# Optimization experiments

Hardware: AMD Instinct MI355X
Metric: run time of the kernel (lower is better)

Reference implementation:

```python
import jax, jax.numpy as jnp
import numpy as np

B, O, T, C_IN, IMG, P, D = 16, 3, 8, 3, 224, 16, 768
HF = IMG // P  # 14x14 conv feature grid
S = 7          # ObjectsCrops output size (SxS per object per frame)


def setup_inputs() -> dict:
    key = jax.random.key(0)
    ks = jax.random.split(key, 6)
    x = jax.random.normal(ks[0], (B, C_IN, T, IMG, IMG), dtype=jnp.float32)
    # metadata: [B, O, T, 4] boxes (x1,y1,x2,y2) in pixel coords within [0,224]
    u = jax.random.uniform(ks[1], (B, O, T, 4), dtype=jnp.float32)
    bx1 = u[..., 0] * 160.0
    by1 = u[..., 1] * 160.0
    bw = 16.0 + u[..., 2] * 48.0
    bh = 16.0 + u[..., 3] * 48.0
    metadata = jnp.stack([bx1, by1, jnp.minimum(bx1 + bw, 224.0), jnp.minimum(by1 + bh, 224.0)], axis=-1)
    proj_w = jax.random.normal(ks[2], (D, C_IN, P, P), dtype=jnp.float32) * 0.02  # Conv3d kernel, tubelet dim (=1) squeezed
    proj_b = jnp.zeros((D,), dtype=jnp.float32)
    box_categories = jax.random.normal(ks[3], (T, O, D), dtype=jnp.float32) * 0.02
    w1 = jax.random.normal(ks[4], (4, D // 2), dtype=jnp.float32) * 0.1   # Linear(4, 384, bias=False)
    w2 = jax.random.normal(ks[5], (D // 2, D), dtype=jnp.float32) * 0.05  # Linear(384, 768, bias=False)
    return dict(x=x, metadata=metadata, proj_w=proj_w, proj_b=proj_b, box_categories=box_categories, w1=w1, w2=w2)


def _roi_crop(feat, boxes):
    # feat: [BT, C, Hf, Wf]; boxes: [BT, O, 4] (x1,y1,x2,y2) in feature-map coords
    BT, C, Hf, Wf = feat.shape
    x1, y1, x2, y2 = (boxes[..., i] for i in range(4))
    cell = (jnp.arange(S, dtype=feat.dtype) + 0.5) / S               # sample cell centers
    ys = y1[..., None] + cell * (y2 - y1)[..., None]                 # [BT,O,S]
    xs = x1[..., None] + cell * (x2 - x1)[..., None]
    yg = jnp.broadcast_to(ys[:, :, :, None], (BT, O, S, S)) - 0.5    # pixel centers at idx+0.5
    xg = jnp.broadcast_to(xs[:, :, None, :], (BT, O, S, S)) - 0.5
    y0f = jnp.floor(yg); x0f = jnp.floor(xg)
    wy = yg - y0f; wx = xg - x0f
    y0 = jnp.clip(y0f.astype(jnp.int32), 0, Hf - 1); y1i = jnp.clip(y0 + 1, 0, Hf - 1)
    x0 = jnp.clip(x0f.astype(jnp.int32), 0, Wf - 1); x1i = jnp.clip(x0 + 1, 0, Wf - 1)
    gather = jax.vmap(lambda fm, yy, xx: fm[:, yy, xx])              # [C,Hf,Wf],[O,S,S] -> [C,O,S,S]
    v00 = gather(feat, y0, x0); v01 = gather(feat, y0, x1i)
    v10 = gather(feat, y1i, x0); v11 = gather(feat, y1i, x1i)
    wy = wy[:, None]; wx = wx[:, None]                               # [BT,1,O,S,S]
    return (v00 * (1 - wy) * (1 - wx) + v01 * (1 - wy) * wx
            + v10 * wy * (1 - wx) + v11 * wy * wx)                   # [BT,C,O,S,S]


def reference(x, metadata, proj_w, proj_b, box_categories, w1, w2):
    Bs = x.shape[0]
    boxes = jnp.transpose(metadata, (0, 2, 1, 3))                    # [B,T,O,4] pixel coords
    # coordinate MLP on normalized boxes + per-(frame,object) category embedding
    box_emb = jax.nn.relu(jax.nn.relu((boxes / 224.0) @ w1) @ w2)    # [B,T,O,D]
    box_emb = box_categories[None] + box_emb
    # Conv3d patch embed: tubelet=1, stride==kernel -> non-overlapping patchify + GEMM
    xp = x.reshape(Bs, C_IN, T, HF, P, HF, P)
    feat = jnp.einsum('bcthpwq,dcpq->btdhw', xp, proj_w) + proj_b[None, None, :, None, None]
    feat = feat.reshape(Bs * T, D, HF, HF)
    fboxes = boxes.reshape(Bs * T, O, 4) * (HF / 224.0)              # boxes in feature coords
    crops = _roi_crop(feat, fboxes).reshape(Bs, T, D, O, S, S)
    xo = jnp.transpose(crops, (0, 3, 2, 1, 4, 5))                    # [B,O,C,T,S,S]
    emb = jnp.transpose(box_emb, (0, 2, 3, 1))                       # [B,O,D,T]
    xo = xo + emb[..., None, None]
    xo = xo.reshape(Bs * O, D, T, S * S)                             # flatten(3) on [N*O,C,T,H,W]
    return jnp.transpose(xo, (0, 2, 3, 1))                           # [B*O, T, S*S, D]
```

## Files before the change

### kernel.cpp

```cpp
#include <hip/hip_runtime.h>
#include <hip/hip_bf16.h>

typedef unsigned int u32;
typedef unsigned short ushort_t;
typedef __bf16 bf16x8 __attribute__((ext_vector_type(8)));
typedef float f32x4 __attribute__((ext_vector_type(4)));
typedef unsigned short ushort8 __attribute__((ext_vector_type(8)));
typedef unsigned short ushort4v __attribute__((ext_vector_type(4)));

#define GM 25088
#define GK 768
#define GN 768

__device__ __forceinline__ ushort_t f2bf(float f) {
    u32 u = __float_as_uint(f);
    u32 r = (u + 0x7FFFu + ((u >> 16) & 1u)) >> 16;
    return (ushort_t)r;
}

__device__ __forceinline__ f32x4 bf2f4(ushort4v u) {
    f32x4 f;
    #pragma unroll
    for (int e = 0; e < 4; ++e) f[e] = __uint_as_float(((u32)u[e]) << 16);
    return f;
}

__device__ __forceinline__ ushort8 cvt8(f32x4 f0, f32x4 f1) {
    ushort8 r;
    r[0] = f2bf(f0[0]); r[1] = f2bf(f0[1]); r[2] = f2bf(f0[2]); r[3] = f2bf(f0[3]);
    r[4] = f2bf(f1[0]); r[5] = f2bf(f1[1]); r[6] = f2bf(f1[2]); r[7] = f2bf(f1[3]);
    return r;
}

__device__ __forceinline__ void load_lds16(const void* g, void* l) {
    __builtin_amdgcn_global_load_lds(
        (const __attribute__((address_space(1))) u32*)g,
        (__attribute__((address_space(3))) u32*)l, 16, 0, 0);
}

__global__ __launch_bounds__(256) void prep(const float* __restrict__ x,
                                            const float* __restrict__ projw,
                                            const float* __restrict__ meta,
                                            const float* __restrict__ w1,
                                            const float* __restrict__ w2,
                                            const float* __restrict__ cats,
                                            ushort_t* __restrict__ Ap,
                                            ushort_t* __restrict__ Wp,
                                            float* __restrict__ emb) {
    __shared__ ushort_t Lsm[3 * 16 * 232];
    __shared__ float H[3][384];
    int bid = blockIdx.x;
    int tid = threadIdx.x;
    if (bid < 1792) {
        int h = bid % 14;
        int t = (bid / 14) % 8;
        int b = bid / 112;
        for (int chunk = tid; chunk < 1344; chunk += 256) {
            int c = chunk / 448;
            int cc = chunk % 448;
            int p = cc / 28;
            int col0 = (cc % 28) * 8;
            const float* s = x + ((size_t)((b * 3 + c) * 8 + t) * 224 + h * 16 + p) * 224 + col0;
            f32x4 f0 = *(const f32x4*)s;
            f32x4 f1 = *(const f32x4*)(s + 4);
            *(ushort8*)&Lsm[(c * 16 + p) * 232 + col0] = cvt8(f0, f1);
        }
        __syncthreads();
        int mbase = ((b * 8 + t) * 14 + h) * 14;
        for (int chunk = tid; chunk < 1344; chunk += 256) {
            int w = chunk / 96;
            int kc = chunk % 96;
            int k0 = kc * 8;
            int c = k0 >> 8;
            int p = (k0 >> 4) & 15;
            int q0 = k0 & 15;
            ushort8 r = *(const ushort8*)&Lsm[(c * 16 + p) * 232 + w * 16 + q0];
            int mm = mbase + w;
            int bytesw = (kc * 16) ^ ((mm & 7) << 4);
            *(ushort8*)(Ap + (size_t)mm * 768 + (bytesw >> 1)) = r;
        }
    } else if (bid < 1828) {
        int g = (bid - 1792) * 256 + tid;
        int n = g / 12;
        int piece = g % 12;
        const float* src = projw + (size_t)n * 768 + piece * 64;
        int xo = (n & 7) << 4;
        ushort_t* dst = Wp + (size_t)n * 768 + piece * 64;
        #pragma unroll
        for (int i = 0; i < 4; ++i) {
            const float* s = src + i * 16;
            f32x4 f0 = *(const f32x4*)(s);
            f32x4 f1 = *(const f32x4*)(s + 4);
            f32x4 f2 = *(const f32x4*)(s + 8);
            f32x4 f3 = *(const f32x4*)(s + 12);
            int b0 = (i * 32) ^ xo;
            int b1 = (i * 32 + 16) ^ xo;
            *(ushort8*)(dst + (b0 >> 1)) = cvt8(f0, f1);
            *(ushort8*)(dst + (b1 >> 1)) = cvt8(f2, f3);
        }
    } else {
        int bb = bid - 1828;
        int bt = bb / 3;
        int dc = bb % 3;
        int b = bt / 8, t = bt % 8;
        for (int idx = tid; idx < 3 * 384; idx += 256) {
            int o = idx / 384, j = idx % 384;
            const float* mp = meta + ((b * 3 + o) * 8 + t) * 4;
            float s = 0.f;
            #pragma unroll
            for (int i = 0; i < 4; ++i) s += (mp[i] * (1.0f / 224.0f)) * w1[i * 384 + j];
            H[o][j] = fmaxf(s, 0.f);
        }
        __syncthreads();
        int d = dc * 256 + tid;
        float acc[3] = {0.f, 0.f, 0.f};
        #pragma unroll 4
        for (int j = 0; j < 384; ++j) {
            float wv = w2[j * 768 + d];
            acc[0] += H[0][j] * wv;
            acc[1] += H[1][j] * wv;
            acc[2] += H[2][j] * wv;
        }
        #pragma unroll
        for (int o = 0; o < 3; ++o) {
            emb[((size_t)bt * 3 + o) * 768 + d] =
                fmaxf(acc[o], 0.f) + cats[(t * 3 + o) * 768 + d];
        }
    }
}

__global__ __launch_bounds__(256) void gemm_bt(const ushort_t* __restrict__ A,
                                               const ushort_t* __restrict__ Bt,
                                               const float* __restrict__ pb,
                                               ushort_t* __restrict__ Cb) {
    __shared__ ushort_t lA[2][128 * 64];
    __shared__ ushort_t lB[2][128 * 64];
    int tid = threadIdx.x;
    int bid = blockIdx.x;
    int wid = (bid & 7) * 147 + (bid >> 3);
    int bm = wid / 6;
    int bn = wid % 6;
    size_t m0 = (size_t)bm * 128, n0 = (size_t)bn * 128;
    int w = tid >> 6, lane = tid & 63;
    int wr = w >> 1, wc = w & 1;
    int r15 = lane & 15;
    int xoU = (lane & 7) << 3;

    f32x4 acc[4][4] = {};

    #define STAGE(buf, kt_)                                                        \
        {                                                                          \
            int k0_ = (kt_) * 64;                                                  \
            _Pragma("unroll")                                                      \
            for (int r = 0; r < 4; ++r) {                                          \
                int cidx = r * 256 + tid;                                          \
                int row = cidx >> 3;                                               \
                int col = (cidx & 7) * 8;                                          \
                load_lds16(A + ((m0 + row) * 768 + k0_ + col), &lA[buf][cidx * 8]);\
            }                                                                      \
            _Pragma("unroll")                                                      \
            for (int r = 0; r < 4; ++r) {                                          \
                int cidx = r * 256 + tid;                                          \
                int row = cidx >> 3;                                               \
                int col = (cidx & 7) * 8;                                          \
                load_lds16(Bt + ((n0 + row) * 768 + k0_ + col), &lB[buf][cidx * 8]);\
            }                                                                      \
        }

    STAGE(0, 0);
    __syncthreads();

    for (int kt = 0; kt < 12; ++kt) {
        int cur = kt & 1;
        if (kt < 11) STAGE(cur ^ 1, kt + 1);
        #pragma unroll
        for (int kk = 0; kk < 2; ++kk) {
            int cs = (kk * 32 + (lane >> 4) * 8) ^ xoU;
            bf16x8 af[4], bfr[4];
            #pragma unroll
            for (int mi = 0; mi < 4; ++mi)
                af[mi] = *(const bf16x8*)&lA[cur][(wr * 64 + mi * 16 + r15) * 64 + cs];
            #pragma unroll
            for (int ni = 0; ni < 4; ++ni)
                bfr[ni] = *(const bf16x8*)&lB[cur][(wc * 64 + ni * 16 + r15) * 64 + cs];
            #pragma unroll
            for (int mi = 0; mi < 4; ++mi)
                #pragma unroll
                for (int ni = 0; ni < 4; ++ni)
                    acc[mi][ni] = __builtin_amdgcn_mfma_f32_16x16x32_bf16(
                        af[mi], bfr[ni], acc[mi][ni], 0, 0, 0);
        }
        __syncthreads();
    }
    #undef STAGE

    int rbase = (lane >> 4) * 4;
    #pragma unroll
    for (int ni = 0; ni < 4; ++ni) {
        size_t col = n0 + wc * 64 + ni * 16 + r15;
        float pbv = pb[col];
        #pragma unroll
        for (int mi = 0; mi < 4; ++mi) {
            size_t row = m0 + wr * 64 + mi * 16 + rbase;
            #pragma unroll
            for (int j = 0; j < 4; ++j) {
                Cb[(row + j) * 768 + col] = f2bf(acc[mi][ni][j] + pbv);
            }
        }
    }
}

__global__ __launch_bounds__(192) void roi_kernel(const float* __restrict__ meta,
                                                  const ushort_t* __restrict__ featB,
                                                  const float* __restrict__ emb,
                                                  float* __restrict__ out) {
    int bid = blockIdx.x;
    int wid = (bid & 7) * 336 + (bid >> 3);
    int i = wid % 7; int r = wid / 7;
    int o = r % 3; r /= 3;
    int t = r % 8;
    int b = r / 8;
    int d = threadIdx.x * 4;

    const float* mp = meta + ((b * 3 + o) * 8 + t) * 4;
    float x1 = mp[0] * (1.f / 16.f);
    float y1 = mp[1] * (1.f / 16.f);
    float x2 = mp[2] * (1.f / 16.f);
    float y2 = mp[3] * (1.f / 16.f);

    float ci = (i + 0.5f) * (1.f / 7.f);
    float yg = y1 + ci * (y2 - y1) - 0.5f;
    float y0f = floorf(yg);
    float wy = yg - y0f;
    int y0 = min(max((int)y0f, 0), 13);
    int y1c = min(y0 + 1, 13);

    int bt = b * 8 + t;
    const ushort_t* fbase = featB + (size_t)bt * 196 * 768;
    const float* ep = emb + ((size_t)bt * 3 + o) * 768;
    f32x4 ev = *(const f32x4*)(ep + d);

    #pragma unroll
    for (int j = 0; j < 7; ++j) {
        float cj = (j + 0.5f) * (1.f / 7.f);
        float xgv = x1 + cj * (x2 - x1) - 0.5f;
        float x0f = floorf(xgv);
        float wx = xgv - x0f;
        int x0 = min(max((int)x0f, 0), 13);
        int x1i = min(x0 + 1, 13);

        f32x4 v00 = bf2f4(*(const ushort4v*)(fbase + ((size_t)y0 * 14 + x0) * 768 + d));
        f32x4 v01 = bf2f4(*(const ushort4v*)(fbase + ((size_t)y0 * 14 + x1i) * 768 + d));
        f32x4 v10 = bf2f4(*(const ushort4v*)(fbase + ((size_t)y1c * 14 + x0) * 768 + d));
        f32x4 v11 = bf2f4(*(const ushort4v*)(fbase + ((size_t)y1c * 14 + x1i) * 768 + d));

        float w00 = (1.f - wy) * (1.f - wx);
        float w01 = (1.f - wy) * wx;
        float w10 = wy * (1.f - wx);
        float w11 = wy * wx;

        f32x4 rr;
        #pragma unroll
        for (int e = 0; e < 4; ++e)
            rr[e] = v00[e] * w00 + v01[e] * w01 + v10[e] * w10 + v11[e] * w11 + ev[e];

        int pp = i * 7 + j;
        *(f32x4*)(out + ((((size_t)(b * 3 + o) * 8 + t) * 49 + pp) * 768 + d)) = rr;
    }
}

extern "C" void kernel_launch(void* const* d_in, const int* in_sizes, int n_in,
                              void* d_out, int out_size, void* d_ws, size_t ws_size,
                              hipStream_t stream) {
    const float* x     = (const float*)d_in[0];
    const float* meta  = (const float*)d_in[1];
    const float* projw = (const float*)d_in[2];
    const float* projb = (const float*)d_in[3];
    const float* cats  = (const float*)d_in[4];
    const float* w1    = (const float*)d_in[5];
    const float* w2    = (const float*)d_in[6];
    float* out = (float*)d_out;

    char* ws = (char*)d_ws;
    const size_t szA  = (size_t)GM * GK * 2;
    const size_t szW  = (size_t)GN * GK * 2;
    const size_t szFB = (size_t)GM * GN * 2;
    ushort_t* Ap    = (ushort_t*)(ws);
    ushort_t* Wp    = (ushort_t*)(ws + szA);
    ushort_t* featB = (ushort_t*)(ws + szA + szW);
    float*    emb   = (float*)(ws + szA + szW + szFB);

    prep<<<2212, 256, 0, stream>>>(x, projw, meta, w1, w2, cats, Ap, Wp, emb);
    gemm_bt<<<1176, 256, 0, stream>>>(Ap, Wp, projb, featB);
    roi_kernel<<<2688, 192, 0, stream>>>(meta, featB, emb, out);
}
```

Before: 243.9 us.

## Split prep into separate kernels and single-buffer the GEMM LDS tiles

The fused prep kernel is split into three launches: A packing, weight packing, and a box-MLP kernel whose w2 loads are batched in groups of 16. The GEMM drops LDS double buffering in favour of a single buffer with two barriers per k-step. This halves GEMM shared memory, which may raise occupancy, but global loads no longer overlap the MFMA work. The split also adds two extra kernel launches.

```diff
diff --git a/kernel.cpp b/kernel.cpp
--- a/kernel.cpp
+++ b/kernel.cpp
@@ -38,94 +38,101 @@
         (__attribute__((address_space(3))) u32*)l, 16, 0, 0);
 }
 
-__global__ __launch_bounds__(256) void prep(const float* __restrict__ x,
-                                            const float* __restrict__ projw,
-                                            const float* __restrict__ meta,
-                                            const float* __restrict__ w1,
-                                            const float* __restrict__ w2,
-                                            const float* __restrict__ cats,
-                                            ushort_t* __restrict__ Ap,
-                                            ushort_t* __restrict__ Wp,
-                                            float* __restrict__ emb) {
+__global__ __launch_bounds__(256) void pack_a(const float* __restrict__ x,
+                                              ushort_t* __restrict__ Ap) {
     __shared__ ushort_t Lsm[3 * 16 * 232];
-    __shared__ float H[3][384];
     int bid = blockIdx.x;
     int tid = threadIdx.x;
-    if (bid < 1792) {
-        int h = bid % 14;
-        int t = (bid / 14) % 8;
-        int b = bid / 112;
-        for (int chunk = tid; chunk < 1344; chunk += 256) {
-            int c = chunk / 448;
-            int cc = chunk % 448;
-            int p = cc / 28;
-            int col0 = (cc % 28) * 8;
-            const float* s = x + ((size_t)((b * 3 + c) * 8 + t) * 224 + h * 16 + p) * 224 + col0;
-            f32x4 f0 = *(const f32x4*)s;
-            f32x4 f1 = *(const f32x4*)(s + 4);
-            *(ushort8*)&Lsm[(c * 16 + p) * 232 + col0] = cvt8(f0, f1);
-        }
-        __syncthreads();
-        int mbase = ((b * 8 + t) * 14 + h) * 14;
-        for (int chunk = tid; chunk < 1344; chunk += 256) {
-            int w = chunk / 96;
-            int kc = chunk % 96;
-            int k0 = kc * 8;
-            int c = k0 >> 8;
-            int p = (k0 >> 4) & 15;
-            int q0 = k0 & 15;
-            ushort8 r = *(const ushort8*)&Lsm[(c * 16 + p) * 232 + w * 16 + q0];
-            int mm = mbase + w;
-            int bytesw = (kc * 16) ^ ((mm & 7) << 4);
-            *(ushort8*)(Ap + (size_t)mm * 768 + (bytesw >> 1)) = r;
-        }
-    } else if (bid < 1828) {
-        int g = (bid - 1792) * 256 + tid;
-        int n = g / 12;
-        int piece = g % 12;
-        const float* src = projw + (size_t)n * 768 + piece * 64;
-        int xo = (n & 7) << 4;
-        ushort_t* dst = Wp + (size_t)n * 768 + piece * 64;
-        #pragma unroll
-        for (int i = 0; i < 4; ++i) {
-            const float* s = src + i * 16;
-            f32x4 f0 = *(const f32x4*)(s);
-            f32x4 f1 = *(const f32x4*)(s + 4);
-            f32x4 f2 = *(const f32x4*)(s + 8);
-            f32x4 f3 = *(const f32x4*)(s + 12);
-            int b0 = (i * 32) ^ xo;
-            int b1 = (i * 32 + 16) ^ xo;
-            *(ushort8*)(dst + (b0 >> 1)) = cvt8(f0, f1);
-            *(ushort8*)(dst + (b1 >> 1)) = cvt8(f2, f3);
-        }
-    } else {
-        int bb = bid - 1828;
-        int bt = bb / 3;
-        int dc = bb % 3;
-        int b = bt / 8, t = bt % 8;
-        for (int idx = tid; idx < 3 * 384; idx += 256) {
-            int o = idx / 384, j = idx % 384;
-            const float* mp = meta + ((b * 3 + o) * 8 + t) * 4;
-            float s = 0.f;
-            #pragma unroll
-            for (int i = 0; i < 4; ++i) s += (mp[i] * (1.0f / 224.0f)) * w1[i * 384 + j];
-            H[o][j] = fmaxf(s, 0.f);
-        }
-        __syncthreads();
-        int d = dc * 256 + tid;
-        float acc[3] = {0.f, 0.f, 0.f};
-        #pragma unroll 4
-        for (int j = 0; j < 384; ++j) {
-            float wv = w2[j * 768 + d];
-            acc[0] += H[0][j] * wv;
-            acc[1] += H[1][j] * wv;
-            acc[2] += H[2][j] * wv;
-        }
-        #pragma unroll
-        for (int o = 0; o < 3; ++o) {
-            emb[((size_t)bt * 3 + o) * 768 + d] =
-                fmaxf(acc[o], 0.f) + cats[(t * 3 + o) * 768 + d];
-        }
+    int h = bid % 14;
+    int t = (bid / 14) % 8;
+    int b = bid / 112;
+    for (int chunk = tid; chunk < 1344; chunk += 256) {
+        int c = chunk / 448;
+        int cc = chunk % 448;
+        int p = cc / 28;
+        int col0 = (cc % 28) * 8;
+        const float* s = x + ((size_t)((b * 3 + c) * 8 + t) * 224 + h * 16 + p) * 224 + col0;
+        f32x4 f0 = *(const f32x4*)s;
+        f32x4 f1 = *(const f32x4*)(s + 4);
+        *(ushort8*)&Lsm[(c * 16 + p) * 232 + col0] = cvt8(f0, f1);
+    }
+    __syncthreads();
+    int mbase = ((b * 8 + t) * 14 + h) * 14;
+    for (int chunk = tid; chunk < 1344; chunk += 256) {
+        int w = chunk / 96;
+        int kc = chunk % 96;
+        int k0 = kc * 8;
+        int c = k0 >> 8;
+        int p = (k0 >> 4) & 15;
+        int q0 = k0 & 15;
+        ushort8 r = *(const ushort8*)&Lsm[(c * 16 + p) * 232 + w * 16 + q0];
+        int mm = mbase + w;
+        int bytesw = (kc * 16) ^ ((mm & 7) << 4);
+        *(ushort8*)(Ap + (size_t)mm * 768 + (bytesw >> 1)) = r;
+    }
+}
+
+__global__ __launch_bounds__(256) void pack_w(const float* __restrict__ projw,
+                                              ushort_t* __restrict__ Wp) {
+    int g = blockIdx.x * 256 + threadIdx.x;
+    int n = g / 12;
+    int piece = g % 12;
+    const float* src = projw + (size_t)n * 768 + piece * 64;
+    int xo = (n & 7) << 4;
+    ushort_t* dst = Wp + (size_t)n * 768 + piece * 64;
+    #pragma unroll
+    for (int i = 0; i < 4; ++i) {
+        const float* s = src + i * 16;
+        f32x4 f0 = *(const f32x4*)(s);
+        f32x4 f1 = *(const f32x4*)(s + 4);
+        f32x4 f2 = *(const f32x4*)(s + 8);
+        f32x4 f3 = *(const f32x4*)(s + 12);
+        int b0 = (i * 32) ^ xo;
+        int b1 = (i * 32 + 16) ^ xo;
+        *(ushort8*)(dst + (b0 >> 1)) = cvt8(f0, f1);
+        *(ushort8*)(dst + (b1 >> 1)) = cvt8(f2, f3);
+    }
+}
+
+__global__ __launch_bounds__(256) void box_mlp(const float* __restrict__ meta,
+                                               const float* __restrict__ w1,
+                                               const float* __restrict__ w2,
+                                               const float* __restrict__ cats,
+                                               float* __restrict__ emb) {
+    __shared__ float H[3][384];
+    int bt = blockIdx.x / 3;
+    int dc = blockIdx.x % 3;
+    int b = bt / 8, t = bt % 8;
+    int tid = threadIdx.x;
+    for (int idx = tid; idx < 3 * 384; idx += 256) {
+        int o = idx / 384, j = idx % 384;
+        const float* mp = meta + ((b * 3 + o) * 8 + t) * 4;
+        float s = 0.f;
+        #pragma unroll
+        for (int i = 0; i < 4; ++i) s += (mp[i] * (1.0f / 224.0f)) * w1[i * 384 + j];
+        H[o][j] = fmaxf(s, 0.f);
+    }
+    __syncthreads();
+    int d = dc * 256 + tid;
+    const float* wp = w2 + d;
+    float acc0 = 0.f, acc1 = 0.f, acc2 = 0.f;
+    #pragma unroll 1
+    for (int j0 = 0; j0 < 384; j0 += 16) {
+        float wv[16];
+        #pragma unroll
+        for (int u = 0; u < 16; ++u) wv[u] = wp[(size_t)(j0 + u) * 768];
+        #pragma unroll
+        for (int u = 0; u < 16; ++u) {
+            acc0 += H[0][j0 + u] * wv[u];
+            acc1 += H[1][j0 + u] * wv[u];
+            acc2 += H[2][j0 + u] * wv[u];
+        }
+    }
+    float a[3] = {acc0, acc1, acc2};
+    #pragma unroll
+    for (int o = 0; o < 3; ++o) {
+        emb[((size_t)bt * 3 + o) * 768 + d] =
+            fmaxf(a[o], 0.f) + cats[(t * 3 + o) * 768 + d];
     }
 }
 
@@ -133,8 +140,8 @@
                                                const ushort_t* __restrict__ Bt,
                                                const float* __restrict__ pb,
                                                ushort_t* __restrict__ Cb) {
-    __shared__ ushort_t lA[2][128 * 64];
-    __shared__ ushort_t lB[2][128 * 64];
+    __shared__ ushort_t lA[128 * 64];
+    __shared__ ushort_t lB[128 * 64];
     int tid = threadIdx.x;
     int bid = blockIdx.x;
     int wid = (bid & 7) * 147 + (bid >> 3);
@@ -148,41 +155,34 @@
 
     f32x4 acc[4][4] = {};
 
-    #define STAGE(buf, kt_)                                                        \
-        {                                                                          \
-            int k0_ = (kt_) * 64;                                                  \
-            _Pragma("unroll")                                                      \
-            for (int r = 0; r < 4; ++r) {                                          \
-                int cidx = r * 256 + tid;                                          \
-                int row = cidx >> 3;                                               \
-                int col = (cidx & 7) * 8;                                          \
-                load_lds16(A + ((m0 + row) * 768 + k0_ + col), &lA[buf][cidx * 8]);\
-            }                                                                      \
-            _Pragma("unroll")                                                      \
-            for (int r = 0; r < 4; ++r) {                                          \
-                int cidx = r * 256 + tid;                                          \
-                int row = cidx >> 3;                                               \
-                int col = (cidx & 7) * 8;                                          \
-                load_lds16(Bt + ((n0 + row) * 768 + k0_ + col), &lB[buf][cidx * 8]);\
-            }                                                                      \
-        }
-
-    STAGE(0, 0);
-    __syncthreads();
-
     for (int kt = 0; kt < 12; ++kt) {
-        int cur = kt & 1;
-        if (kt < 11) STAGE(cur ^ 1, kt + 1);
+        int k0 = kt * 64;
+        __syncthreads();
+        #pragma unroll
+        for (int r = 0; r < 4; ++r) {
+            int cidx = r * 256 + tid;
+            int row = cidx >> 3;
+            int col = (cidx & 7) * 8;
+            load_lds16(A + ((m0 + row) * 768 + k0 + col), &lA[(size_t)cidx * 8]);
+        }
+        #pragma unroll
+        for (int r = 0; r < 4; ++r) {
+            int cidx = r * 256 + tid;
+            int row = cidx >> 3;
+            int col = (cidx & 7) * 8;
+            load_lds16(Bt + ((n0 + row) * 768 + k0 + col), &lB[(size_t)cidx * 8]);
+        }
+        __syncthreads();
         #pragma unroll
         for (int kk = 0; kk < 2; ++kk) {
             int cs = (kk * 32 + (lane >> 4) * 8) ^ xoU;
             bf16x8 af[4], bfr[4];
             #pragma unroll
             for (int mi = 0; mi < 4; ++mi)
-                af[mi] = *(const bf16x8*)&lA[cur][(wr * 64 + mi * 16 + r15) * 64 + cs];
+                af[mi] = *(const bf16x8*)&lA[(wr * 64 + mi * 16 + r15) * 64 + cs];
             #pragma unroll
             for (int ni = 0; ni < 4; ++ni)
-                bfr[ni] = *(const bf16x8*)&lB[cur][(wc * 64 + ni * 16 + r15) * 64 + cs];
+                bfr[ni] = *(const bf16x8*)&lB[(wc * 64 + ni * 16 + r15) * 64 + cs];
             #pragma unroll
             for (int mi = 0; mi < 4; ++mi)
                 #pragma unroll
@@ -190,9 +190,7 @@
                     acc[mi][ni] = __builtin_amdgcn_mfma_f32_16x16x32_bf16(
                         af[mi], bfr[ni], acc[mi][ni], 0, 0, 0);
         }
-        __syncthreads();
-    }
-    #undef STAGE
+    }
 
     int rbase = (lane >> 4) * 4;
     #pragma unroll
@@ -290,7 +288,9 @@
     ushort_t* featB = (ushort_t*)(ws + szA + szW);
     float*    emb   = (float*)(ws + szA + szW + szFB);
 
-    prep<<<2212, 256, 0, stream>>>(x, projw, meta, w1, w2, cats, Ap, Wp, emb);
+    pack_a<<<1792, 256, 0, stream>>>(x, Ap);
+    pack_w<<<36, 256, 0, stream>>>(projw, Wp);
+    box_mlp<<<384, 256, 0, stream>>>(meta, w1, w2, cats, emb);
     gemm_bt<<<1176, 256, 0, stream>>>(Ap, Wp, projb, featB);
     roi_kernel<<<2688, 192, 0, stream>>>(meta, featB, emb, out);
 }
```

After: 225.8 us. 7.4% less time.
